# Kernel optimization log

Measured on AMD Instinct MI355X. Metric: run time of the kernel, lower is better.

## Reference

```python
import jax, jax.numpy as jnp
import numpy as np

N_NODES = 50000
N_EDGES = 800000
D_IN, D_HID, D_OUT = 16, 64, 16
N_BLOCKS = 4


def setup_inputs() -> dict:
    key = jax.random.key(0)
    ks = jax.random.split(key, 12)
    s = 0.05  # small init scale to keep sum-aggregation over 4 blocks stable
    return {
        "x": jax.random.normal(ks[0], (N_NODES, D_IN), jnp.float32),
        "lframes": jax.random.normal(ks[1], (N_NODES, 4, 4), jnp.float32),
        "edge_index": jax.random.randint(ks[2], (2, N_EDGES), 0, N_NODES, jnp.int64),
        "lin_in_w": jax.random.normal(ks[3], (D_IN, D_HID), jnp.float32) * s,
        "lin_in_b": jnp.zeros((D_HID,), jnp.float32),
        # per-block mlp1: Linear(2D->D), ReLU, Linear(D->D), ReLU, Linear(D->D)
        "w0": jax.random.normal(ks[4], (N_BLOCKS, 2 * D_HID, D_HID), jnp.float32) * s,
        "b0": jnp.zeros((N_BLOCKS, D_HID), jnp.float32),
        "w1": jax.random.normal(ks[5], (N_BLOCKS, D_HID, D_HID), jnp.float32) * s,
        "b1": jnp.zeros((N_BLOCKS, D_HID), jnp.float32),
        "w2": jax.random.normal(ks[6], (N_BLOCKS, D_HID, D_HID), jnp.float32) * s,
        "b2": jnp.zeros((N_BLOCKS, D_HID), jnp.float32),
        "lin_out_w": jax.random.normal(ks[7], (D_HID, D_OUT), jnp.float32) * s,
        "lin_out_b": jnp.zeros((D_OUT,), jnp.float32),
    }


def reference(x, lframes, edge_index, lin_in_w, lin_in_b,
              w0, b0, w1, b1, w2, b2, lin_out_w, lin_out_b):
    src = edge_index[0]  # x_j (source / neighbor)
    dst = edge_index[1]  # x_i (target / aggregation node)
    h = x @ lin_in_w + lin_in_b  # [N, D]
    for k in range(N_BLOCKS):
        # message: cat((x_j, x_i)) -> mlp1 ; mlp2 is Identity (num_layers_mlp2=0)
        m = jnp.concatenate((h[src], h[dst]), axis=-1)  # [E, 2D]
        m = jax.nn.relu(m @ w0[k] + b0[k])
        m = jax.nn.relu(m @ w1[k] + b1[k])
        m = m @ w2[k] + b2[k]  # [E, D]
        # aggregate: scatter-add at target node
        h = jax.ops.segment_sum(m, dst, num_segments=N_NODES)
    return h @ lin_out_w + lin_out_b  # [N, D_OUT]
```

## Files before the change

### kernel.cpp

```cpp
#include <hip/hip_runtime.h>
#include <hip/hip_bf16.h>

#define N_NODES 50000
#define N_EDGES 800000
#define D_IN    16
#define D_HID   64
#define D_OUT   16
#define NCHUNK  ((N_NODES + 255) / 256)
#define TMAX    100352
#define GE8     ((N_EDGES / 8 + 255) / 256)
#define GH      ((N_NODES * D_HID + 255) / 256)
#define SCAP    48
#define NSLOTV  (N_NODES * SCAP / 8)

typedef __hip_bfloat16 bf16;
typedef _Float16 f16;
typedef _Float16 f16x8 __attribute__((ext_vector_type(8)));
typedef float    f32x4 __attribute__((ext_vector_type(4)));
typedef _Float16 f16x8a __attribute__((ext_vector_type(8), may_alias));
typedef int      i32x4 __attribute__((ext_vector_type(4)));
typedef unsigned short u16x8a __attribute__((ext_vector_type(8), may_alias));
typedef float    f32x4a __attribute__((ext_vector_type(4), may_alias));

__device__ __forceinline__ float b2f(bf16 v) { return __bfloat162float(v); }
__device__ __forceinline__ float bfb(unsigned short u) {
    union { unsigned u; float f; } z; z.u = (unsigned)u << 16; return z.f;
}
__device__ __forceinline__ int clampn(int v) {
    return v < 0 ? 0 : (v >= N_NODES ? N_NODES - 1 : v);
}
__device__ __forceinline__ float rdf(const void* p, long i, int isbf) {
    return isbf ? b2f(((const bf16*)p)[i]) : ((const float*)p)[i];
}
__device__ __forceinline__ f16x8 relu8(f16x8 v) {
#pragma unroll
    for (int j = 0; j < 8; j++) v[j] = v[j] > (f16)0 ? v[j] : (f16)0;
    return v;
}
__device__ __forceinline__ int sbase(int m) {
    return (m & 0xFFFFF) * SCAP + ((m >> 25) & 3) * 16;
}

__global__ __launch_bounds__(256) void k_detect(const unsigned short* __restrict__ xw,
                                                const int* __restrict__ ei,
                                                int* __restrict__ flags,
                                                int* __restrict__ cursor,
                                                unsigned short* __restrict__ slots,
                                                unsigned short* __restrict__ psrc_us)
{
    int gtid = blockIdx.x * 256 + threadIdx.x;
    if (gtid < N_NODES) cursor[gtid] = 0;
    const int dpat = (int)0xC350C350;
    const i32x4 fillv = {dpat, dpat, dpat, dpat};
#pragma unroll
    for (int k = 0; k < 6; k++) {
        int q = k * (NCHUNK * 256) + gtid;
        if (q < NSLOTV) ((i32x4*)slots)[q] = fillv;
    }
    if (blockIdx.x == 0 && threadIdx.x < 64)
        psrc_us[(size_t)N_NODES * 64 + threadIdx.x] = 0xFC00u;
    if (blockIdx.x == 0 && threadIdx.x == 0) {
        int inband = 0;
        for (int j = 0; j < 256; j++) {
            unsigned short w = xw[2 * j];
            int e = (w >> 7) & 0xFF;
            if ((w & 0x7FFF) == 0 || (e >= 100 && e <= 140)) inband++;
        }
        flags[0] = (inband >= 192) ? 1 : 0;
        int z = 1;
        for (int j = 1; j < 128; j += 2) z &= (ei[j] == 0) ? 1 : 0;
        flags[1] = z;
    }
}

__global__ __launch_bounds__(256) void k_scatter8(const int* __restrict__ flags,
                                                  const int* __restrict__ eidx,
                                                  int* __restrict__ cursor,
                                                  unsigned short* __restrict__ slots)
{
    int base = (blockIdx.x * 256 + threadIdx.x) * 8;
    if (base >= N_EDGES) return;
    const int strd = flags[1] ? 2 : 1;
    const long dbase = flags[1] ? (long)(2 * N_EDGES) : (long)N_EDGES;
    int d[8], s[8], pos[8], cnt = min(8, N_EDGES - base);
#pragma unroll
    for (int j = 0; j < 8; j++)
        if (j < cnt) {
            d[j] = clampn(eidx[dbase + (long)(base + j) * strd]);
            s[j] = clampn(eidx[(long)(base + j) * strd]);
        }
#pragma unroll
    for (int j = 0; j < 8; j++)
        if (j < cnt) pos[j] = atomicAdd(&cursor[d[j]], 1);
#pragma unroll
    for (int j = 0; j < 8; j++)
        if (j < cnt && pos[j] < SCAP)
            slots[d[j] * SCAP + pos[j]] = (unsigned short)s[j];
}

__global__ __launch_bounds__(256) void k_prep(const int* __restrict__ flags,
                                              const void* __restrict__ gw0,
                                              const void* __restrict__ gw1,
                                              const void* __restrict__ gw2,
                                              f16* __restrict__ wfrag,
                                              const void* __restrict__ x,
                                              const void* __restrict__ liw,
                                              const void* __restrict__ lib,
                                              float* __restrict__ h,
                                              const void* __restrict__ gb1,
                                              const void* __restrict__ gb2,
                                              float* __restrict__ cpad)
{
    const int isbf = flags[0];
    const int bid = blockIdx.x;
    if (bid < 32) {
        int idx = bid * 256 + threadIdx.x;
        int kb = idx >> 11, rem = idx & 2047;
        int slot = rem >> 6, lane = rem & 63;
        int lm = lane & 15, quad = lane >> 4;
        f16* outp = wfrag + (long)idx * 8;
        if (slot < 16) {
            int c = slot >> 2, q = slot & 3;
            long base = (long)kb * 2 * D_HID * D_HID;
#pragma unroll
            for (int j = 0; j < 8; j++)
                outp[j] = (f16)rdf(gw0, base + (long)(c * 32 + quad * 8 + j) * 64 + q * 16 + lm, isbf);
        } else {
            const void* gw = (slot < 24) ? gw1 : gw2;
            int s = (slot < 24) ? slot - 16 : slot - 24;
            int c = s >> 2, q = s & 3;
            long base = (long)kb * D_HID * D_HID;
#pragma unroll
            for (int j = 0; j < 8; j++)
                outp[j] = (f16)rdf(gw, base + (long)(c * 32 + quad * 8 + j) * 64 + q * 16 + lm, isbf);
        }
    } else if (bid < 32 + GH) {
        int idx = (bid - 32) * 256 + threadIdx.x;
        if (idx >= N_NODES * D_HID) return;
        int n = idx >> 6, c = idx & 63;
        float acc, wr[16], xr[16];
        if (isbf) {
            const unsigned short* xp = (const unsigned short*)x + (long)n * 16;
            u16x8a x0 = *(const u16x8a*)xp, x1 = *(const u16x8a*)(xp + 8);
#pragma unroll
            for (int i = 0; i < 8; i++) { xr[i] = bfb(x0[i]); xr[8 + i] = bfb(x1[i]); }
            const unsigned short* wq = (const unsigned short*)liw;
#pragma unroll
            for (int i = 0; i < 16; i++) wr[i] = bfb(wq[i * 64 + c]);
            acc = bfb(((const unsigned short*)lib)[c]);
        } else {
            const float* xp = (const float*)x + (long)n * 16;
#pragma unroll
            for (int q = 0; q < 4; q++) {
                f32x4a v = *(const f32x4a*)(xp + q * 4);
#pragma unroll
                for (int j = 0; j < 4; j++) xr[q * 4 + j] = v[j];
            }
            const float* wq = (const float*)liw;
#pragma unroll
            for (int i = 0; i < 16; i++) wr[i] = wq[i * 64 + c];
            acc = ((const float*)lib)[c];
        }
#pragma unroll
        for (int i = 0; i < 16; i++) acc += xr[i] * wr[i];
        h[idx] = acc;
    } else {
        int t = threadIdx.x;
        int k = t >> 6, j = t & 63;
        float acc = rdf(gb2, (long)k * 64 + j, isbf);
        for (int i = 0; i < 64; i++) {
            float zi = (float)(f16)fmaxf(rdf(gb1, (long)k * 64 + i, isbf), 0.f);
            float wi = (float)(f16)rdf(gw2, (long)k * 4096 + (long)i * 64 + j, isbf);
            acc += zi * wi;
        }
        cpad[k * 64 + j] = acc;
    }
}

__global__ __launch_bounds__(256) void k_scan1(const int* __restrict__ deg,
                                               int* __restrict__ bsum_t)
{
    __shared__ int rt[256];
    const int t = threadIdx.x;
    int i = blockIdx.x * 256 + t;
    int v = (i < N_NODES) ? deg[i] : 0;
    rt[t] = min((v + 15) >> 4, 3);
    __syncthreads();
    for (int d = 128; d > 0; d >>= 1) {
        if (t < d) rt[t] += rt[t + d];
        __syncthreads();
    }
    if (t == 0) bsum_t[blockIdx.x] = rt[0];
}

__global__ __launch_bounds__(256) void k_scan2(const int* __restrict__ bsum_t,
                                               int* __restrict__ boff_t,
                                               int* __restrict__ tot_t)
{
    __shared__ int st_[256];
    const int t = threadIdx.x;
    st_[t] = (t < NCHUNK) ? bsum_t[t] : 0;
    __syncthreads();
    for (int d = 1; d < 256; d <<= 1) {
        int vt = (t >= d) ? st_[t - d] : 0;
        __syncthreads();
        st_[t] += vt;
        __syncthreads();
    }
    if (t < NCHUNK) boff_t[t] = (t == 0) ? 0 : st_[t - 1];
    if (t == NCHUNK - 1) tot_t[0] = st_[t];
}

__global__ __launch_bounds__(256) void k_scan3(const int* __restrict__ deg,
                                               const int* __restrict__ boff_t,
                                               int* __restrict__ toff,
                                               int* __restrict__ tmeta)
{
    __shared__ int st_[256];
    const int t = threadIdx.x;
    int i = blockIdx.x * 256 + t;
    int v = (i < N_NODES) ? deg[i] : 0;
    int w = min((v + 15) >> 4, 3);
    st_[t] = w;
    __syncthreads();
    for (int d = 1; d < 256; d <<= 1) {
        int ut = (t >= d) ? st_[t - d] : 0;
        __syncthreads();
        st_[t] += ut;
        __syncthreads();
    }
    if (i < N_NODES) {
        int exT = boff_t[blockIdx.x] + st_[t] - w;
        toff[i] = exT;
        for (int j = 0; j < w; j++)
            tmeta[exT + j] = i | (min(16, v - 16 * j) << 20) | (j << 25);
    }
}

#define HP_ST 72

__global__ __launch_bounds__(256) void k_proj(
    const int* __restrict__ flags, float* hio,
    const f16* __restrict__ wfrag, const void* __restrict__ gb0,
    const int* __restrict__ deg,
    f16* __restrict__ psrc, f16* __restrict__ pdst, int kblk)
{
    __shared__ f16 hL_s[4][16 * HP_ST];

    const int tid  = threadIdx.x;
    const int isbf = flags[0];
    const int wv = tid >> 6, ln = tid & 63;
    const int lm = ln & 15, quad = ln >> 4;
    f16* hL = hL_s[wv];

    const int g = blockIdx.x * 4 + wv;
    if (g >= N_NODES / 16) return;
    const int n0 = g * 16;

    const f16* wb = wfrag + (long)kblk * 32 * 64 * 8;

#pragma unroll
    for (int i = 0; i < 16; i++) {
        int idx = i * 64 + ln;
        hL[(idx >> 6) * HP_ST + (idx & 63)] = (f16)hio[(long)n0 * 64 + idx];
    }
#pragma unroll
    for (int i = 0; i < 16; i++)
        if (deg[n0 + i] == 0) hio[(long)(n0 + i) * 64 + ln] = 0.f;

    f16x8 a[2];
#pragma unroll
    for (int c = 0; c < 2; c++)
        a[c] = *(const f16x8a*)&hL[lm * HP_ST + c * 32 + quad * 8];

    f32x4 accS[4], accD[4];
#pragma unroll
    for (int q = 0; q < 4; q++) {
        float bd = rdf(gb0, (long)kblk * 64 + q * 16 + lm, isbf);
        accS[q] = (f32x4){0.f, 0.f, 0.f, 0.f};
        accD[q] = (f32x4){bd, bd, bd, bd};
    }
#pragma unroll
    for (int c = 0; c < 2; c++)
#pragma unroll
        for (int q = 0; q < 4; q++) {
            f16x8 bs = *(const f16x8a*)&wb[(((c + 0) * 4 + q) * 64 + ln) * 8];
            f16x8 bd = *(const f16x8a*)&wb[(((c + 2) * 4 + q) * 64 + ln) * 8];
            accS[q] = __builtin_amdgcn_mfma_f32_16x16x32_f16(a[c], bs, accS[q], 0, 0, 0);
            accD[q] = __builtin_amdgcn_mfma_f32_16x16x32_f16(a[c], bd, accD[q], 0, 0, 0);
        }
#pragma unroll
    for (int q = 0; q < 4; q++)
#pragma unroll
        for (int r = 0; r < 4; r++) {
            long o = (long)(n0 + quad * 4 + r) * 64 + q * 16 + lm;
            psrc[o] = (f16)accS[q][r];
            pdst[o] = (f16)accD[q][r];
        }
}

#define Y_ST 72

__global__ __launch_bounds__(256) void k_edge_tile(
    const int* __restrict__ flags,
    const unsigned short* __restrict__ slots, const int* __restrict__ tmeta,
    const int* __restrict__ toff,
    const f16* __restrict__ psrc, const f16* __restrict__ pdst,
    float* __restrict__ hout,
    const f16* __restrict__ wfrag, const void* __restrict__ gb1,
    const void* __restrict__ gb2, const float* __restrict__ cpad, int kblk)
{
    __shared__ f16 y_s[4][16 * Y_ST];

    const int tid  = threadIdx.x;
    const int isbf = flags[0];
    const int wv = tid >> 6, ln = tid & 63;
    const int lm = ln & 15, quad = ln >> 4;
    const int sub = ln & 7, eh = ln >> 3;
    f16* y = y_s[wv];

    const f16* wb = wfrag + (long)kblk * 32 * 64 * 8;
    f16x8 bw1[2][4], bw2[2][4];
#pragma unroll
    for (int c = 0; c < 2; c++)
#pragma unroll
        for (int q = 0; q < 4; q++) {
            bw1[c][q] = *(const f16x8a*)&wb[((16 + c * 4 + q) * 64 + ln) * 8];
            bw2[c][q] = *(const f16x8a*)&wb[((24 + c * 4 + q) * 64 + ln) * 8];
        }
    float bias1[4], bias2[4], cp[4];
#pragma unroll
    for (int q = 0; q < 4; q++) {
        bias1[q] = rdf(gb1, (long)kblk * 64 + q * 16 + lm, isbf);
        bias2[q] = rdf(gb2, (long)kblk * 64 + q * 16 + lm, isbf);
        cp[q]    = cpad[kblk * 64 + q * 16 + lm];
    }

    const int T  = toff[N_NODES];
    const int W  = gridDim.x * 4;
    const int gw = blockIdx.x * 4 + wv;
    int t0 = (int)((long)gw * T / W);
    int t1 = (int)((long)(gw + 1) * T / W);
    if (t0 > 0)
        while (t0 < T && (tmeta[t0] & 0xFFFFF) == (tmeta[t0 - 1] & 0xFFFFF)) t0++;
    if (t1 > 0)
        while (t1 < T && (tmeta[t1] & 0xFFFFF) == (tmeta[t1 - 1] & 0xFFFFF)) t1++;
    if (t0 >= t1) return;

    int mA = tmeta[t0];
    int mB = tmeta[min(t0 + 1, T - 1)];
    int mC = tmeta[min(t0 + 2, T - 1)];
    int bA = sbase(mA), bB = sbase(mB);
    int sAa = slots[bA + eh], sAb = slots[bA + 8 + eh];
    int sBa = slots[bB + eh], sBb = slots[bB + 8 + eh];
    f16x8 psAa = *(const f16x8a*)&psrc[(long)sAa * 64 + sub * 8];
    f16x8 psAb = *(const f16x8a*)&psrc[(long)sAb * 64 + sub * 8];
    f16x8 pdA  = *(const f16x8a*)&pdst[(long)(mA & 0xFFFFF) * 64 + sub * 8];

    float accn[4] = {0.f, 0.f, 0.f, 0.f};

    for (int tt = t0; tt < t1; ++tt) {
        const int mD = tmeta[min(tt + 3, T - 1)];
        const int bC = sbase(mC);
        const int sCa = slots[bC + eh], sCb = slots[bC + 8 + eh];
        f16x8 psBa = *(const f16x8a*)&psrc[(long)sBa * 64 + sub * 8];
        f16x8 psBb = *(const f16x8a*)&psrc[(long)sBb * 64 + sub * 8];
        f16x8 pdB  = *(const f16x8a*)&pdst[(long)(mB & 0xFFFFF) * 64 + sub * 8];

        *(f16x8a*)&y[eh * Y_ST + sub * 8]       = relu8(psAa + pdA);
        *(f16x8a*)&y[(8 + eh) * Y_ST + sub * 8] = relu8(psAb + pdA);

        f16x8 a1[2];
        a1[0] = *(const f16x8a*)&y[lm * Y_ST + quad * 8];
        a1[1] = *(const f16x8a*)&y[lm * Y_ST + 32 + quad * 8];
        f32x4 acc[4];
#pragma unroll
        for (int q = 0; q < 4; q++)
            acc[q] = (f32x4){bias1[q], bias1[q], bias1[q], bias1[q]};
#pragma unroll
        for (int c = 0; c < 2; c++)
#pragma unroll
            for (int q = 0; q < 4; q++)
                acc[q] = __builtin_amdgcn_mfma_f32_16x16x32_f16(a1[c], bw1[c][q], acc[q], 0, 0, 0);
#pragma unroll
        for (int q = 0; q < 4; q++)
#pragma unroll
            for (int r = 0; r < 4; r++)
                y[(quad * 4 + r) * Y_ST + q * 16 + lm] = (f16)fmaxf(acc[q][r], 0.f);

        f16x8 a2[2];
        a2[0] = *(const f16x8a*)&y[lm * Y_ST + quad * 8];
        a2[1] = *(const f16x8a*)&y[lm * Y_ST + 32 + quad * 8];
#pragma unroll
        for (int q = 0; q < 4; q++)
            acc[q] = (f32x4){bias2[q], bias2[q], bias2[q], bias2[q]};
#pragma unroll
        for (int c = 0; c < 2; c++)
#pragma unroll
            for (int q = 0; q < 4; q++)
                acc[q] = __builtin_amdgcn_mfma_f32_16x16x32_f16(a2[c], bw2[c][q], acc[q], 0, 0, 0);

#pragma unroll
        for (int q = 0; q < 4; q++)
#pragma unroll
            for (int r = 0; r < 4; r++)
                accn[q] += acc[q][r];

        const int curn = mA & 0xFFFFF;
        const int nxt  = (tt + 1 < t1) ? (mB & 0xFFFFF) : -1;
        if (nxt != curn) {
            const float npad = (float)(16 - ((mA >> 20) & 31));
#pragma unroll
            for (int q = 0; q < 4; q++) {
                float v = accn[q];
                v += __shfl_xor(v, 16, 64);
                v += __shfl_xor(v, 32, 64);
                if (quad == 0) hout[(long)curn * 64 + q * 16 + lm] = v - npad * cp[q];
                accn[q] = 0.f;
            }
        }

        mA = mB; mB = mC; mC = mD;
        sBa = sCa; sBb = sCb;
        psAa = psBa; psAb = psBb; pdA = pdB;
    }
}

__global__ __launch_bounds__(256) void k_lin_out(const int* __restrict__ flags,
                                                 const float* __restrict__ h,
                                                 const void* __restrict__ w,
                                                 const void* __restrict__ b,
                                                 float* __restrict__ out)
{
    __shared__ float wl[D_HID * D_OUT];
    __shared__ float bl[D_OUT];
    const int isbf = flags[0];
    const int t = threadIdx.x;
    for (int k = t; k < D_HID * D_OUT; k += 256) wl[k] = rdf(w, k, isbf);
    if (t < D_OUT) bl[t] = rdf(b, t, isbf);
    __syncthreads();

    int idx = blockIdx.x * 256 + t;
    if (idx >= N_NODES * D_OUT) return;
    int n = idx >> 4, c = idx & 15;
    const float* hr = h + (long)n * D_HID;
    float acc = bl[c];
#pragma unroll
    for (int i = 0; i < 16; i++) {
        f32x4a v = *(const f32x4a*)(hr + i * 4);
        acc += v[0] * wl[(i * 4 + 0) * 16 + c] + v[1] * wl[(i * 4 + 1) * 16 + c]
             + v[2] * wl[(i * 4 + 2) * 16 + c] + v[3] * wl[(i * 4 + 3) * 16 + c];
    }
    out[idx] = acc;
}

extern "C" void kernel_launch(void* const* d_in, const int* in_sizes, int n_in,
                              void* d_out, int out_size, void* d_ws, size_t ws_size,
                              hipStream_t stream)
{
    const void* x    = d_in[0];
    const int*  ei   = (const int*)d_in[2];
    const void* liw  = d_in[3];
    const void* lib  = d_in[4];
    const void* w0   = d_in[5];
    const void* b0   = d_in[6];
    const void* w1   = d_in[7];
    const void* b1   = d_in[8];
    const void* w2   = d_in[9];
    const void* b2   = d_in[10];
    const void* low  = d_in[11];
    const void* lob  = d_in[12];
    float* out = (float*)d_out;

    char* wp = (char*)d_ws;
    int*   flags  = (int*)wp;                 wp += 256;
    float* hA     = (float*)wp;               wp += (size_t)N_NODES * D_HID * 4;
    f16*   Psrc   = (f16*)wp;                 wp += ((size_t)N_NODES + 1) * D_HID * 2;
    f16*   Pdst   = (f16*)wp;                 wp += (size_t)N_NODES * D_HID * 2;
    f16*   wfrag  = (f16*)wp;                 wp += (size_t)4 * 32 * 64 * 8 * 2;
    float* cpad   = (float*)wp;               wp += (size_t)4 * 64 * 4;
    int*   cursor = (int*)wp;                 wp += (size_t)N_NODES * 4;
    int*   bsum_t = (int*)wp;                 wp += 256 * 4;
    int*   boff_t = (int*)wp;                 wp += 256 * 4;
    int*   tmeta  = (int*)wp;                 wp += (size_t)TMAX * 4;
    unsigned short* slots = (unsigned short*)wp; wp += (size_t)N_NODES * SCAP * 2;
    int*   toff   = (int*)wp;

    k_detect<<<NCHUNK, 256, 0, stream>>>((const unsigned short*)x, ei, flags,
                                         cursor, slots, (unsigned short*)Psrc);
    k_scatter8<<<GE8, 256, 0, stream>>>(flags, ei, cursor, slots);
    k_prep<<<32 + GH + 1, 256, 0, stream>>>(flags, w0, w1, w2, wfrag,
                                            x, liw, lib, hA, b1, b2, cpad);

    k_scan1<<<NCHUNK, 256, 0, stream>>>(cursor, bsum_t);
    k_scan2<<<1, 256, 0, stream>>>(bsum_t, boff_t, toff + N_NODES);
    k_scan3<<<NCHUNK, 256, 0, stream>>>(cursor, boff_t, toff, tmeta);

    for (int k = 0; k < 4; k++) {
        k_proj<<<(N_NODES / 16 + 3) / 4, 256, 0, stream>>>(flags, hA, wfrag, b0,
                                                           cursor, Psrc, Pdst, k);
        k_edge_tile<<<2048, 256, 0, stream>>>(flags, slots, tmeta, toff,
                                              Psrc, Pdst, hA, wfrag, b1, b2,
                                              cpad, k);
    }

    k_lin_out<<<(N_NODES * D_OUT + 255) / 256, 256, 0, stream>>>(flags, hA, low, lob, out);
}
```

Before: 414.7 us.

## Fuse edge scatter into prep kernel and restructure edge-tile MFMA epilogue

Moves the edge-bucketing scatter into the k_prep launch as extra blocks, removing one kernel launch. In the edge tile kernel, the first MFMA now takes its operands in swapped order so each lane's outputs can be packed into f16x4 vector stores to shared memory, replacing scattered scalar stores. The second-layer bias is no longer added per tile; it is folded into the per-node flush as tile-count times b2. Results accumulate directly in the MFMA accumulators across tiles, and biases are staged in shared memory. This trades a small extra flush computation and shared-memory setup for fewer per-tile ALU adds and fewer LDS stores.

```diff
diff --git a/kernel.cpp b/kernel.cpp
--- a/kernel.cpp
+++ b/kernel.cpp
@@ -16,8 +16,10 @@
 typedef __hip_bfloat16 bf16;
 typedef _Float16 f16;
 typedef _Float16 f16x8 __attribute__((ext_vector_type(8)));
+typedef _Float16 f16x4 __attribute__((ext_vector_type(4)));
 typedef float    f32x4 __attribute__((ext_vector_type(4)));
 typedef _Float16 f16x8a __attribute__((ext_vector_type(8), may_alias));
+typedef _Float16 f16x4a __attribute__((ext_vector_type(4), may_alias));
 typedef int      i32x4 __attribute__((ext_vector_type(4)));
 typedef unsigned short u16x8a __attribute__((ext_vector_type(8), may_alias));
 typedef float    f32x4a __attribute__((ext_vector_type(4), may_alias));
@@ -35,6 +37,11 @@
 __device__ __forceinline__ f16x8 relu8(f16x8 v) {
 #pragma unroll
     for (int j = 0; j < 8; j++) v[j] = v[j] > (f16)0 ? v[j] : (f16)0;
+    return v;
+}
+__device__ __forceinline__ f16x4 relu4(f16x4 v) {
+#pragma unroll
+    for (int j = 0; j < 4; j++) v[j] = v[j] > (f16)0 ? v[j] : (f16)0;
     return v;
 }
 __device__ __forceinline__ int sbase(int m) {
@@ -73,36 +80,14 @@
     }
 }
 
-__global__ __launch_bounds__(256) void k_scatter8(const int* __restrict__ flags,
-                                                  const int* __restrict__ eidx,
-                                                  int* __restrict__ cursor,
-                                                  unsigned short* __restrict__ slots)
-{
-    int base = (blockIdx.x * 256 + threadIdx.x) * 8;
-    if (base >= N_EDGES) return;
-    const int strd = flags[1] ? 2 : 1;
-    const long dbase = flags[1] ? (long)(2 * N_EDGES) : (long)N_EDGES;
-    int d[8], s[8], pos[8], cnt = min(8, N_EDGES - base);
-#pragma unroll
-    for (int j = 0; j < 8; j++)
-        if (j < cnt) {
-            d[j] = clampn(eidx[dbase + (long)(base + j) * strd]);
-            s[j] = clampn(eidx[(long)(base + j) * strd]);
-        }
-#pragma unroll
-    for (int j = 0; j < 8; j++)
-        if (j < cnt) pos[j] = atomicAdd(&cursor[d[j]], 1);
-#pragma unroll
-    for (int j = 0; j < 8; j++)
-        if (j < cnt && pos[j] < SCAP)
-            slots[d[j] * SCAP + pos[j]] = (unsigned short)s[j];
-}
-
 __global__ __launch_bounds__(256) void k_prep(const int* __restrict__ flags,
                                               const void* __restrict__ gw0,
                                               const void* __restrict__ gw1,
                                               const void* __restrict__ gw2,
                                               f16* __restrict__ wfrag,
+                                              const int* __restrict__ eidx,
+                                              int* __restrict__ cursor,
+                                              unsigned short* __restrict__ slots,
                                               const void* __restrict__ x,
                                               const void* __restrict__ liw,
                                               const void* __restrict__ lib,
@@ -134,8 +119,27 @@
             for (int j = 0; j < 8; j++)
                 outp[j] = (f16)rdf(gw, base + (long)(c * 32 + quad * 8 + j) * 64 + q * 16 + lm, isbf);
         }
-    } else if (bid < 32 + GH) {
-        int idx = (bid - 32) * 256 + threadIdx.x;
+    } else if (bid < 32 + GE8) {
+        int base = ((bid - 32) * 256 + threadIdx.x) * 8;
+        if (base >= N_EDGES) return;
+        const int strd = flags[1] ? 2 : 1;
+        const long dbase = flags[1] ? (long)(2 * N_EDGES) : (long)N_EDGES;
+        int d[8], s[8], pos[8], cnt = min(8, N_EDGES - base);
+#pragma unroll
+        for (int j = 0; j < 8; j++)
+            if (j < cnt) {
+                d[j] = clampn(eidx[dbase + (long)(base + j) * strd]);
+                s[j] = clampn(eidx[(long)(base + j) * strd]);
+            }
+#pragma unroll
+        for (int j = 0; j < 8; j++)
+            if (j < cnt) pos[j] = atomicAdd(&cursor[d[j]], 1);
+#pragma unroll
+        for (int j = 0; j < 8; j++)
+            if (j < cnt && pos[j] < SCAP)
+                slots[d[j] * SCAP + pos[j]] = (unsigned short)s[j];
+    } else if (bid < 32 + GE8 + GH) {
+        int idx = (bid - 32 - GE8) * 256 + threadIdx.x;
         if (idx >= N_NODES * D_HID) return;
         int n = idx >> 6, c = idx & 63;
         float acc, wr[16], xr[16];
@@ -311,6 +315,7 @@
     const void* __restrict__ gb2, const float* __restrict__ cpad, int kblk)
 {
     __shared__ f16 y_s[4][16 * Y_ST];
+    __shared__ float b1L[64], b2L[64], cpL[64];
 
     const int tid  = threadIdx.x;
     const int isbf = flags[0];
@@ -319,6 +324,11 @@
     const int sub = ln & 7, eh = ln >> 3;
     f16* y = y_s[wv];
 
+    if (tid < 64)       b1L[tid]       = rdf(gb1, (long)kblk * 64 + tid, isbf);
+    else if (tid < 128) b2L[tid - 64]  = rdf(gb2, (long)kblk * 64 + (tid - 64), isbf);
+    else if (tid < 192) cpL[tid - 128] = cpad[kblk * 64 + (tid - 128)];
+    __syncthreads();
+
     const f16* wb = wfrag + (long)kblk * 32 * 64 * 8;
     f16x8 bw1[2][4], bw2[2][4];
 #pragma unroll
@@ -328,13 +338,6 @@
             bw1[c][q] = *(const f16x8a*)&wb[((16 + c * 4 + q) * 64 + ln) * 8];
             bw2[c][q] = *(const f16x8a*)&wb[((24 + c * 4 + q) * 64 + ln) * 8];
         }
-    float bias1[4], bias2[4], cp[4];
-#pragma unroll
-    for (int q = 0; q < 4; q++) {
-        bias1[q] = rdf(gb1, (long)kblk * 64 + q * 16 + lm, isbf);
-        bias2[q] = rdf(gb2, (long)kblk * 64 + q * 16 + lm, isbf);
-        cp[q]    = cpad[kblk * 64 + q * 16 + lm];
-    }
 
     const int T  = toff[N_NODES];
     const int W  = gridDim.x * 4;
@@ -357,7 +360,9 @@
     f16x8 psAb = *(const f16x8a*)&psrc[(long)sAb * 64 + sub * 8];
     f16x8 pdA  = *(const f16x8a*)&pdst[(long)(mA & 0xFFFFF) * 64 + sub * 8];
 
-    float accn[4] = {0.f, 0.f, 0.f, 0.f};
+    f32x4 accv[4];
+#pragma unroll
+    for (int q = 0; q < 4; q++) accv[q] = (f32x4){0.f, 0.f, 0.f, 0.f};
 
     for (int tt = t0; tt < t1; ++tt) {
         const int mD = tmeta[min(tt + 3, T - 1)];
@@ -373,50 +378,46 @@
         f16x8 a1[2];
         a1[0] = *(const f16x8a*)&y[lm * Y_ST + quad * 8];
         a1[1] = *(const f16x8a*)&y[lm * Y_ST + 32 + quad * 8];
-        f32x4 acc[4];
+        f32x4 acc1[4];
 #pragma unroll
         for (int q = 0; q < 4; q++)
-            acc[q] = (f32x4){bias1[q], bias1[q], bias1[q], bias1[q]};
+            acc1[q] = *(const f32x4a*)&b1L[q * 16 + quad * 4];
 #pragma unroll
         for (int c = 0; c < 2; c++)
 #pragma unroll
             for (int q = 0; q < 4; q++)
-                acc[q] = __builtin_amdgcn_mfma_f32_16x16x32_f16(a1[c], bw1[c][q], acc[q], 0, 0, 0);
-#pragma unroll
-        for (int q = 0; q < 4; q++)
-#pragma unroll
-            for (int r = 0; r < 4; r++)
-                y[(quad * 4 + r) * Y_ST + q * 16 + lm] = (f16)fmaxf(acc[q][r], 0.f);
+                acc1[q] = __builtin_amdgcn_mfma_f32_16x16x32_f16(bw1[c][q], a1[c], acc1[q], 0, 0, 0);
+#pragma unroll
+        for (int q = 0; q < 4; q++) {
+            f16x4 pk = { (f16)acc1[q][0], (f16)acc1[q][1],
+                         (f16)acc1[q][2], (f16)acc1[q][3] };
+            *(f16x4a*)&y[lm * Y_ST + q * 16 + quad * 4] = relu4(pk);
+        }
 
         f16x8 a2[2];
         a2[0] = *(const f16x8a*)&y[lm * Y_ST + quad * 8];
         a2[1] = *(const f16x8a*)&y[lm * Y_ST + 32 + quad * 8];
 #pragma unroll
-        for (int q = 0; q < 4; q++)
-            acc[q] = (f32x4){bias2[q], bias2[q], bias2[q], bias2[q]};
-#pragma unroll
         for (int c = 0; c < 2; c++)
 #pragma unroll
             for (int q = 0; q < 4; q++)
-                acc[q] = __builtin_amdgcn_mfma_f32_16x16x32_f16(a2[c], bw2[c][q], acc[q], 0, 0, 0);
-
-#pragma unroll
-        for (int q = 0; q < 4; q++)
-#pragma unroll
-            for (int r = 0; r < 4; r++)
-                accn[q] += acc[q][r];
+                accv[q] = __builtin_amdgcn_mfma_f32_16x16x32_f16(a2[c], bw2[c][q], accv[q], 0, 0, 0);
 
         const int curn = mA & 0xFFFFF;
         const int nxt  = (tt + 1 < t1) ? (mB & 0xFFFFF) : -1;
         if (nxt != curn) {
             const float npad = (float)(16 - ((mA >> 20) & 31));
+            const float nt16 = (float)((((mA >> 25) & 3) + 1) * 16);
 #pragma unroll
             for (int q = 0; q < 4; q++) {
-                float v = accn[q];
+                float v = accv[q][0] + accv[q][1] + accv[q][2] + accv[q][3];
                 v += __shfl_xor(v, 16, 64);
                 v += __shfl_xor(v, 32, 64);
-                if (quad == 0) hout[(long)curn * 64 + q * 16 + lm] = v - npad * cp[q];
-                accn[q] = 0.f;
+                if (quad == 0) {
+                    const int f = q * 16 + lm;
+                    hout[(long)curn * 64 + f] = v + nt16 * b2L[f] - npad * cpL[f];
+                }
+                accv[q] = (f32x4){0.f, 0.f, 0.f, 0.f};
             }
         }
 
@@ -488,9 +489,9 @@
 
     k_detect<<<NCHUNK, 256, 0, stream>>>((const unsigned short*)x, ei, flags,
                                          cursor, slots, (unsigned short*)Psrc);
-    k_scatter8<<<GE8, 256, 0, stream>>>(flags, ei, cursor, slots);
-    k_prep<<<32 + GH + 1, 256, 0, stream>>>(flags, w0, w1, w2, wfrag,
-                                            x, liw, lib, hA, b1, b2, cpad);
+    k_prep<<<32 + GE8 + GH + 1, 256, 0, stream>>>(flags, w0, w1, w2, wfrag,
+                                                  ei, cursor, slots,
+                                                  x, liw, lib, hA, b1, b2, cpad);
 
     k_scan1<<<NCHUNK, 256, 0, stream>>>(cursor, bsum_t);
     k_scan2<<<1, 256, 0, stream>>>(bsum_t, boff_t, toff + N_NODES);
```

Measured after the change: 397.0 us. 1.04x faster.
